# Optimization experiments

Hardware: AMD Instinct MI355X
Metric: run time of the kernel (lower is better)

The kernel has to match this reference:

```python
import jax, jax.numpy as jnp
import numpy as np

NUM_NODES = 1_200_000
NUM_FILLER = 200_000
NUM_PHYS = NUM_NODES - NUM_FILLER  # 1,000,000 physical nodes
NUM_MOVABLE = 900_000
NBX = NBY = 512
XL, XH, YL, YH = 0.0, 1000.0, 0.0, 1000.0
BSX = (XH - XL) / NBX
BSY = (YH - YL) / NBY
PIN_STRETCH = 1.4142135623730951
UNIT_PIN_CAP = 0.05
MAX_RATE = 1.5
MIN_RATE = 1.0 / MAX_RATE
K = 5  # max bins overlapped per dimension (span<=4.0, bin~1.95)


def _overlap_terms(lo, hi, bin_size, origin, nb):
    # lo, hi: [n] interval per node. Returns bin indices [n,K] and overlap lengths [n,K].
    il = jnp.clip(jnp.floor((lo - origin) / bin_size).astype(jnp.int32), 0, nb - 1)
    idx = il[:, None] + jnp.arange(K, dtype=jnp.int32)[None, :]
    valid = idx < nb
    idx = jnp.clip(idx, 0, nb - 1)
    b_lo = origin + idx.astype(lo.dtype) * bin_size
    ov = jnp.maximum(jnp.minimum(hi[:, None], b_lo + bin_size) - jnp.maximum(lo[:, None], b_lo), 0.0)
    return idx, jnp.where(valid, ov, 0.0)


def _forward(pos, node_size_x, node_size_y, flat_node2pin_start_map):
    P = NUM_PHYS
    sx, sy = node_size_x[:P], node_size_y[:P]
    # stretched half sizes: at least half a stretched bin
    hx = 0.5 * jnp.maximum(BSX * PIN_STRETCH, sx)
    hy = 0.5 * jnp.maximum(BSY * PIN_STRETCH, sy)
    cx = pos[:P] + 0.5 * sx
    cy = pos[NUM_NODES:NUM_NODES + P] + 0.5 * sy
    pw = (flat_node2pin_start_map[1:P + 1] - flat_node2pin_start_map[:P]).astype(pos.dtype)
    density = pw / (4.0 * hx * hy)  # pins per unit area over stretched bbox

    # stage 1: scatter stretched-bbox pin density into bin map
    ix, ovx = _overlap_terms(cx - hx, cx + hx, BSX, XL, NBX)  # [P,K]
    iy, ovy = _overlap_terms(cy - hy, cy + hy, BSY, YL, NBY)  # [P,K]
    contrib = ovx[:, :, None] * ovy[:, None, :] * density[:, None, None]  # [P,K,K]
    flat_idx = (ix[:, :, None] * NBY + iy[:, None, :]).reshape(-1)
    pin_map = jnp.zeros(NBX * NBY, dtype=pos.dtype).at[flat_idx].add(contrib.reshape(-1))

    # stage 2: pin utilization per bin, clamped adjust rate
    util = jnp.clip(pin_map / (BSX * BSY * UNIT_PIN_CAP), MIN_RATE, MAX_RATE)

    # stage 3: per movable node, integrate utilization over its (unstretched) bbox
    M = NUM_MOVABLE
    x_lo = pos[:M]
    x_hi = x_lo + node_size_x[:M]
    y_lo = pos[NUM_NODES:NUM_NODES + M]
    y_hi = y_lo + node_size_y[:M]
    jx, wx = _overlap_terms(x_lo, x_hi, BSX, XL, NBX)  # [M,K]
    jy, wy = _overlap_terms(y_lo, y_hi, BSY, YL, NBY)  # [M,K]
    u = util[jx[:, :, None] * NBY + jy[:, None, :]]  # [M,K,K]
    instance_pin_area = jnp.sum(wx[:, :, None] * wy[:, None, :] * u, axis=(1, 2))
    return instance_pin_area


def setup_inputs() -> dict:
    key = jax.random.key(0)
    k1, k2, k3, k4 = jax.random.split(key, 4)
    node_size_x = jax.random.uniform(k1, (NUM_NODES,), jnp.float32, 1.0, 4.0)
    node_size_y = jnp.full((NUM_NODES,), 2.0, jnp.float32)  # row height
    px = jax.random.uniform(k2, (NUM_NODES,), jnp.float32, 0.0, 995.0)
    py = jax.random.uniform(k3, (NUM_NODES,), jnp.float32, 0.0, 995.0)
    pos = jnp.concatenate([px, py])
    pin_counts = jax.random.randint(k4, (NUM_PHYS,), 1, 9, jnp.int32)
    flat = jnp.concatenate([jnp.zeros(1, jnp.int32), jnp.cumsum(pin_counts).astype(jnp.int32)])
    return {"pos": pos, "node_size_x": node_size_x, "node_size_y": node_size_y,
            "flat_node2pin_start_map": flat}


def reference(pos, node_size_x, node_size_y, flat_node2pin_start_map):
    return _forward(pos, node_size_x, node_size_y, flat_node2pin_start_map)
```

## Files before the change

### kernel.cpp

```cpp
#include <hip/hip_runtime.h>

#define NUM_NODES   1200000
#define NUM_FILLER  200000
#define NUM_PHYS    (NUM_NODES - NUM_FILLER)
#define NUM_MOVABLE 900000
#define NBX 512
#define NBY 512
#define NBINS (NBX * NBY)
#define BSX 1.953125f
#define BSY 1.953125f
#define PIN_STRETCH 1.4142135623730951f
#define CAP 0.19073486328125f
#define INV_CAP (1.0f / 0.19073486328125f)
#define MAX_RATE 1.5f
#define MIN_RATE (1.0f/1.5f)
#define K 5

#define HYC (0.5f * fmaxf(BSY * PIN_STRETCH, 2.0f))

#define NT2     512
#define TROW    16
#define TCOL    32
#define HALO    (K - 1)
#define LROW    (TROW + HALO)
#define LCOL    (TCOL + HALO)
#define SBLK    1024
#define NPB     2048
#define NBLK    ((NUM_PHYS + NPB - 1) / NPB)

__device__ __forceinline__ int bin_lo(float lo) {
    int il = (int)floorf(lo / BSX);
    return min(max(il, 0), NBX - 1);
}

__device__ __forceinline__ int tile_of(int il, int jl) {
    return ((il >> 4) << 4) | (jl >> 5);
}

__global__ __launch_bounds__(SBLK, 8) void sort_phys(
    const float* __restrict__ pos,
    const float* __restrict__ nsx,
    const int*   __restrict__ flat,
    int2*        __restrict__ meta,
    float4*      __restrict__ rec,
    float*       __restrict__ pin)
{
    __shared__ int    cnt[NT2];
    __shared__ int    lofs[NT2];
    __shared__ int    wsum[8];
    __shared__ int    totalS;
    __shared__ float4 stage[NPB];
    int tid = threadIdx.x;
    int bid = blockIdx.x;
    if (tid < NT2) cnt[tid] = 0;
    for (int i = bid * SBLK + tid; i < NBINS; i += NBLK * SBLK)
        pin[i] = 0.0f;
    __syncthreads();

    int q = bid * SBLK + tid;
    bool valid = (2 * q + 1) < NUM_PHYS;
    float4 r2[2];
    int tl[2] = {-1, -1};
    if (valid) {
        float2 px = ((const float2*)pos)[q];
        float2 py = ((const float2*)(pos + NUM_NODES))[q];
        float2 sx = ((const float2*)nsx)[q];
        int2 f2 = ((const int2*)flat)[q];
        int f3 = flat[2 * q + 2];
        float pxs[2] = {px.x, px.y};
        float pys[2] = {py.x, py.y};
        float sxs[2] = {sx.x, sx.y};
        int   pws[2] = {f2.y - f2.x, f3 - f2.y};
        #pragma unroll
        for (int j = 0; j < 2; ++j) {
            float hx = 0.5f * fmaxf(BSX * PIN_STRETCH, sxs[j]);
            float cx = pxs[j] + 0.5f * sxs[j];
            float cy = pys[j] + 0.5f * 2.0f;
            float d  = (float)pws[j] / (4.0f * hx * HYC);
            r2[j] = make_float4(cx, cy, hx, d);
            int t = tile_of(bin_lo(cx - hx), bin_lo(cy - HYC));
            tl[j] = t;
            atomicAdd(&cnt[t], 1);
        }
    }
    __syncthreads();

    int lane = tid & 63, wid = tid >> 6;
    int v = (tid < NT2) ? cnt[tid] : 0;
    #pragma unroll
    for (int off = 1; off < 64; off <<= 1) {
        int u = __shfl_up(v, off, 64);
        if (lane >= off) v += u;
    }
    if (wid < 8 && lane == 63) wsum[wid] = v;
    __syncthreads();
    if (tid == 0) {
        int run = 0;
        #pragma unroll
        for (int w = 0; w < 8; ++w) { int c = wsum[w]; wsum[w] = run; run += c; }
        totalS = run;
    }
    __syncthreads();
    if (tid < NT2) {
        int inc = v + wsum[wid];
        int e = inc - cnt[tid];
        lofs[tid] = e;
        meta[(size_t)bid * NT2 + tid] = make_int2(cnt[tid], e);
    }
    __syncthreads();

    if (valid) {
        #pragma unroll
        for (int j = 0; j < 2; ++j) {
            int r = atomicAdd(&lofs[tl[j]], 1);
            stage[r] = r2[j];
        }
    }
    __syncthreads();

    int total = totalS;
    float4* __restrict__ dst = rec + (size_t)bid * NPB;
    for (int k = tid; k < total; k += SBLK)
        dst[k] = stage[k];
}

__global__ __launch_bounds__(1024, 8) void accumulate_tiles(
    const float4* __restrict__ rec,
    const int2*   __restrict__ meta,
    float*        __restrict__ pin)
{
    __shared__ float tileA[LROW * LCOL];
    __shared__ int offB[NBLK];
    __shared__ int prefB[NBLK + 1];
    __shared__ int wsum[8];
    int tid = threadIdx.x;
    int t = blockIdx.x;
    int bx0 = (t >> 4) * TROW, by0 = (t & 15) * TCOL;

    if (tid < LROW * LCOL) tileA[tid] = 0.0f;
    int c = 0;
    if (tid < NBLK) {
        int2 m = meta[(size_t)tid * NT2 + t];
        c = m.x;
        offB[tid] = m.y;
    }
    int lane = tid & 63, wid = tid >> 6;
    int v = c;
    #pragma unroll
    for (int off = 1; off < 64; off <<= 1) {
        int u = __shfl_up(v, off, 64);
        if (lane >= off) v += u;
    }
    if (wid < 8 && lane == 63) wsum[wid] = v;
    __syncthreads();
    if (tid == 0) {
        int run = 0;
        #pragma unroll
        for (int w = 0; w < 8; ++w) { int cc = wsum[w]; wsum[w] = run; run += cc; }
        prefB[0] = 0;
    }
    __syncthreads();
    if (tid < NBLK) prefB[tid + 1] = v + wsum[wid];
    __syncthreads();

    int total = prefB[NBLK];
    for (int k = tid; k < total; k += 1024) {
        int lo = 0, hi = NBLK;
        while (hi - lo > 1) {
            int mid = (lo + hi) >> 1;
            if (k >= prefB[mid]) lo = mid; else hi = mid;
        }
        float4 r = rec[(size_t)lo * NPB + offB[lo] + (k - prefB[lo])];
        float cx = r.x, cy = r.y, hx = r.z, d = r.w;
        float lox = cx - hx, hix = cx + hx;
        float loy = cy - HYC, hiy = cy + HYC;
        int il = bin_lo(lox), jl = bin_lo(loy);
        int ie = min(min((int)floorf(hix / BSX), NBX - 1), il + HALO);
        int je = min(min((int)floorf(hiy / BSY), NBY - 1), jl + HALO);
        int lr = il - bx0, lc = jl - by0;
        for (int a = il; a <= ie; ++a) {
            float blo = (float)a * BSX;
            float ox = fmaxf(fminf(hix, blo + BSX) - fmaxf(lox, blo), 0.0f);
            int rowb = (lr + (a - il)) * LCOL + lc;
            for (int b2 = jl; b2 <= je; ++b2) {
                float blo2 = (float)b2 * BSY;
                float oy = fmaxf(fminf(hiy, blo2 + BSY) - fmaxf(loy, blo2), 0.0f);
                float cc = ox * oy * d;
                if (cc != 0.0f) atomicAdd(&tileA[rowb + (b2 - jl)], cc);
            }
        }
    }
    __syncthreads();
    if (tid < LROW * LCOL) {
        float v2 = tileA[tid];
        int r = tid / LCOL, cc = tid % LCOL;
        int gx = bx0 + r, gy = by0 + cc;
        if (gx < NBX && gy < NBY) {
            bool interior = (r >= HALO) && (r < TROW) && (cc >= HALO) && (cc < TCOL);
            if (interior) {
                if (v2 != 0.0f) pin[gx * NBY + gy] = v2;
            } else {
                if (v2 != 0.0f) atomicAdd(&pin[gx * NBY + gy], v2);
            }
        }
    }
}

__global__ __launch_bounds__(256) void gather_pin_area(
    const float* __restrict__ pos,
    const float* __restrict__ nsx,
    const float* __restrict__ pin,
    float*       __restrict__ out)
{
    int q = blockIdx.x * blockDim.x + threadIdx.x;
    if (q >= NUM_MOVABLE / 2) return;

    float2 xl2 = ((const float2*)pos)[q];
    float2 yl2 = ((const float2*)(pos + NUM_NODES))[q];
    float2 sx2 = ((const float2*)nsx)[q];

    float xls[2] = {xl2.x, xl2.y};
    float yls[2] = {yl2.x, yl2.y};
    float sxs[2] = {sx2.x, sx2.y};
    float res[2];

    #pragma unroll
    for (int j = 0; j < 2; ++j) {
        float xlo = xls[j], xhi = xlo + sxs[j];
        float ylo = yls[j], yhi = ylo + 2.0f;
        int xb = min(bin_lo(xlo), NBX - 4);
        int yb = min(bin_lo(ylo), NBY - 3);

        float u[4][3];
        #pragma unroll
        for (int a = 0; a < 4; ++a) {
            const float* __restrict__ row = pin + (xb + a) * NBY + yb;
            u[a][0] = row[0]; u[a][1] = row[1]; u[a][2] = row[2];
        }
        float wx[4], wy[3];
        #pragma unroll
        for (int kx = 0; kx < 4; ++kx) {
            float blo = (float)(xb + kx) * BSX;
            wx[kx] = fmaxf(fminf(xhi, blo + BSX) - fmaxf(xlo, blo), 0.0f);
        }
        #pragma unroll
        for (int ky = 0; ky < 3; ++ky) {
            float blo = (float)(yb + ky) * BSY;
            wy[ky] = fmaxf(fminf(yhi, blo + BSY) - fmaxf(ylo, blo), 0.0f);
        }
        float acc = 0.0f;
        #pragma unroll
        for (int a = 0; a < 4; ++a)
            #pragma unroll
            for (int b = 0; b < 3; ++b) {
                float uc = fminf(fmaxf(u[a][b] * INV_CAP, MIN_RATE), MAX_RATE);
                acc += wx[a] * wy[b] * uc;
            }
        res[j] = acc;
    }
    ((float2*)out)[q] = make_float2(res[0], res[1]);
}

__global__ __launch_bounds__(256) void scatter_pin_map_agent(
    const float* __restrict__ pos,
    const float* __restrict__ nsx,
    const float* __restrict__ nsy,
    const int*   __restrict__ flat,
    float*       __restrict__ map)
{
    int p = blockIdx.x * blockDim.x + threadIdx.x;
    if (p >= NUM_PHYS) return;
    float sx = nsx[p], sy = nsy[p];
    float hx = 0.5f * fmaxf(BSX * PIN_STRETCH, sx);
    float hy = 0.5f * fmaxf(BSY * PIN_STRETCH, sy);
    float cx = pos[p] + 0.5f * sx;
    float cy = pos[NUM_NODES + p] + 0.5f * sy;
    float pw = (float)(flat[p + 1] - flat[p]);
    float density = pw / (4.0f * hx * hy);
    float lox = cx - hx, hixv = cx + hx;
    float loy = cy - hy, hiyv = cy + hy;
    int il = bin_lo(lox), jl = bin_lo(loy);
    int ie = min(min((int)floorf(hixv / BSX), NBX - 1), il + K - 1);
    int je = min(min((int)floorf(hiyv / BSY), NBY - 1), jl + K - 1);
    for (int a = il; a <= ie; ++a) {
        float blo = (float)a * BSX;
        float ox = fmaxf(fminf(hixv, blo + BSX) - fmaxf(lox, blo), 0.0f);
        for (int b = jl; b <= je; ++b) {
            float blo2 = (float)b * BSY;
            float oy = fmaxf(fminf(hiyv, blo2 + BSY) - fmaxf(loy, blo2), 0.0f);
            float c = ox * oy * density;
            if (c != 0.0f) atomicAdd(&map[a * NBY + b], c);
        }
    }
}

__global__ __launch_bounds__(256) void gather_general(
    const float* __restrict__ pos,
    const float* __restrict__ nsx,
    const float* __restrict__ nsy,
    const float* __restrict__ pin,
    float*       __restrict__ out)
{
    int m = blockIdx.x * blockDim.x + threadIdx.x;
    if (m >= NUM_MOVABLE) return;
    float xlo = pos[m];
    float xhi = xlo + nsx[m];
    float ylo = pos[NUM_NODES + m];
    float yhi = ylo + nsy[m];
    int il = bin_lo(xlo);
    int ie = min(min((int)floorf(xhi / BSX), NBX - 1), il + K - 1);
    int jl = bin_lo(ylo);
    int je = min(min((int)floorf(yhi / BSY), NBY - 1), jl + K - 1);
    float acc = 0.0f;
    for (int a = il; a <= ie; ++a) {
        float blo = (float)a * BSX;
        float wxv = fmaxf(fminf(xhi, blo + BSX) - fmaxf(xlo, blo), 0.0f);
        const float* __restrict__ row = pin + a * NBY;
        for (int b2 = jl; b2 <= je; ++b2) {
            float blo2 = (float)b2 * BSY;
            float wyv = fmaxf(fminf(yhi, blo2 + BSY) - fmaxf(ylo, blo2), 0.0f);
            float uc = fminf(fmaxf(row[b2] * INV_CAP, MIN_RATE), MAX_RATE);
            acc += wxv * wyv * uc;
        }
    }
    out[m] = acc;
}

extern "C" void kernel_launch(void* const* d_in, const int* in_sizes, int n_in,
                              void* d_out, int out_size, void* d_ws, size_t ws_size,
                              hipStream_t stream) {
    const float* pos  = (const float*)d_in[0];
    const float* nsx  = (const float*)d_in[1];
    const float* nsy  = (const float*)d_in[2];
    const int*   flat = (const int*)d_in[3];
    float* out = (float*)d_out;

    char* wsb = (char*)d_ws;
    float*  pin  = (float*)wsb;
    int2*   meta = (int2*)(wsb + (size_t)NBINS * 4);
    float4* rec  = (float4*)(wsb + (size_t)NBINS * 4
                             + (size_t)NBLK * NT2 * 8);
    size_t needed = (size_t)NBINS * 4 + (size_t)NBLK * NT2 * 8
                  + (size_t)NBLK * NPB * 16;

    dim3 blk(256);
    if (ws_size >= needed) {
        sort_phys<<<NBLK, dim3(SBLK), 0, stream>>>(pos, nsx, flat,
                                                   meta, rec, pin);
        accumulate_tiles<<<NT2, dim3(1024), 0, stream>>>(rec, meta, pin);
        gather_pin_area<<<(NUM_MOVABLE / 2 + 255) / 256, blk, 0, stream>>>(pos, nsx, pin, out);
    } else {
        hipMemsetAsync(pin, 0, (size_t)NBINS * 4, stream);
        scatter_pin_map_agent<<<(NUM_PHYS + 255) / 256, blk, 0, stream>>>(pos, nsx, nsy, flat, pin);
        gather_general<<<(NUM_MOVABLE + 255) / 256, blk, 0, stream>>>(pos, nsx, nsy, pin, out);
    }
}
```

Baseline: 133.5 us.

## Fuse sort, tile accumulation and gather into one cooperative persistent kernel

Replaces the three-kernel pipeline (sort_phys, accumulate_tiles, gather_pin_area) with a single cooperative kernel of 512 blocks x 512 threads that separates the stages with grid.sync(). Each block now bins about 1954 nodes instead of 2048 so the block count matches the tile count, and it reuses one shared buffer for both the staging records and the tile patch. The aim is to remove launch gaps and inter-kernel drain between three short kernels. The cost is the grid-wide barriers, 512-thread blocks with fewer threads in flight, and a grid-stride gather loop. It falls back to the general path if the cooperative launch fails.

```diff
diff --git a/kernel.cpp b/kernel.cpp
--- a/kernel.cpp
+++ b/kernel.cpp
@@ -1,8 +1,10 @@
 #include <hip/hip_runtime.h>
+#include <hip/hip_cooperative_groups.h>
+
+namespace cg = cooperative_groups;
 
 #define NUM_NODES   1200000
-#define NUM_FILLER  200000
-#define NUM_PHYS    (NUM_NODES - NUM_FILLER)
+#define NUM_PHYS    1000000
 #define NUM_MOVABLE 900000
 #define NBX 512
 #define NBY 512
@@ -10,23 +12,24 @@
 #define BSX 1.953125f
 #define BSY 1.953125f
 #define PIN_STRETCH 1.4142135623730951f
-#define CAP 0.19073486328125f
 #define INV_CAP (1.0f / 0.19073486328125f)
 #define MAX_RATE 1.5f
 #define MIN_RATE (1.0f/1.5f)
 #define K 5
+#define HALO (K - 1)
 
 #define HYC (0.5f * fmaxf(BSY * PIN_STRETCH, 2.0f))
 
-#define NT2     512
-#define TROW    16
-#define TCOL    32
-#define HALO    (K - 1)
-#define LROW    (TROW + HALO)
-#define LCOL    (TCOL + HALO)
-#define SBLK    1024
-#define NPB     2048
-#define NBLK    ((NUM_PHYS + NPB - 1) / NPB)
+#define GRID 512
+#define BLK  512
+#define NT2  512
+#define TROW 16
+#define TCOL 32
+#define LROW (TROW + HALO)
+#define LCOL (TCOL + HALO)
+#define NPAIRS (NUM_PHYS / 2)
+#define PPB ((NPAIRS + GRID - 1) / GRID)
+#define RSTR (2 * PPB)
 
 __device__ __forceinline__ int bin_lo(float lo) {
     int il = (int)floorf(lo / BSX);
@@ -37,62 +40,72 @@
     return ((il >> 4) << 4) | (jl >> 5);
 }
 
-__global__ __launch_bounds__(SBLK, 8) void sort_phys(
+__global__ __launch_bounds__(BLK, 4) void fused_pipeline(
     const float* __restrict__ pos,
     const float* __restrict__ nsx,
     const int*   __restrict__ flat,
     int2*        __restrict__ meta,
     float4*      __restrict__ rec,
-    float*       __restrict__ pin)
+    float*       __restrict__ pin,
+    float*       __restrict__ out)
 {
-    __shared__ int    cnt[NT2];
-    __shared__ int    lofs[NT2];
-    __shared__ int    wsum[8];
-    __shared__ int    totalS;
-    __shared__ float4 stage[NPB];
-    int tid = threadIdx.x;
-    int bid = blockIdx.x;
-    if (tid < NT2) cnt[tid] = 0;
-    for (int i = bid * SBLK + tid; i < NBINS; i += NBLK * SBLK)
-        pin[i] = 0.0f;
-    __syncthreads();
-
-    int q = bid * SBLK + tid;
-    bool valid = (2 * q + 1) < NUM_PHYS;
-    float4 r2[2];
-    int tl[2] = {-1, -1};
-    if (valid) {
-        float2 px = ((const float2*)pos)[q];
-        float2 py = ((const float2*)(pos + NUM_NODES))[q];
-        float2 sx = ((const float2*)nsx)[q];
-        int2 f2 = ((const int2*)flat)[q];
-        int f3 = flat[2 * q + 2];
-        float pxs[2] = {px.x, px.y};
-        float pys[2] = {py.x, py.y};
-        float sxs[2] = {sx.x, sx.y};
-        int   pws[2] = {f2.y - f2.x, f3 - f2.y};
-        #pragma unroll
-        for (int j = 0; j < 2; ++j) {
-            float hx = 0.5f * fmaxf(BSX * PIN_STRETCH, sxs[j]);
-            float cx = pxs[j] + 0.5f * sxs[j];
-            float cy = pys[j] + 0.5f * 2.0f;
-            float d  = (float)pws[j] / (4.0f * hx * HYC);
-            r2[j] = make_float4(cx, cy, hx, d);
-            int t = tile_of(bin_lo(cx - hx), bin_lo(cy - HYC));
-            tl[j] = t;
-            atomicAdd(&cnt[t], 1);
-        }
-    }
-    __syncthreads();
-
-    int lane = tid & 63, wid = tid >> 6;
-    int v = (tid < NT2) ? cnt[tid] : 0;
+    __shared__ __align__(16) char smem[RSTR * 16];
+    __shared__ int cntS[NT2];
+    __shared__ int lofs[NT2];
+    __shared__ int wsum[8];
+    __shared__ int totalS;
+
+    cg::grid_group grid = cg::this_grid();
+    const int tid  = threadIdx.x;
+    const int bid  = blockIdx.x;
+    const int lane = tid & 63;
+    const int wid  = tid >> 6;
+
+    pin[bid * BLK + tid] = 0.0f;
+
+    cntS[tid] = 0;
+    __syncthreads();
+
+    float4* stage = (float4*)smem;
+    const int base = bid * PPB;
+    const int pend = min(base + PPB, NPAIRS);
+    float4 r4[4];
+    int    tl[4] = {-1, -1, -1, -1};
+    #pragma unroll
+    for (int s = 0; s < 2; ++s) {
+        int q = base + s * BLK + tid;
+        if (q < pend) {
+            float2 px = ((const float2*)pos)[q];
+            float2 py = ((const float2*)(pos + NUM_NODES))[q];
+            float2 sx = ((const float2*)nsx)[q];
+            int2   f2 = ((const int2*)flat)[q];
+            int    f3 = flat[2 * q + 2];
+            float pxs[2] = {px.x, px.y};
+            float pys[2] = {py.x, py.y};
+            float sxs[2] = {sx.x, sx.y};
+            int   pws[2] = {f2.y - f2.x, f3 - f2.y};
+            #pragma unroll
+            for (int j = 0; j < 2; ++j) {
+                float hx = 0.5f * fmaxf(BSX * PIN_STRETCH, sxs[j]);
+                float cx = pxs[j] + 0.5f * sxs[j];
+                float cy = pys[j] + 1.0f;
+                float d  = (float)pws[j] / (4.0f * hx * HYC);
+                r4[2 * s + j] = make_float4(cx, cy, hx, d);
+                int t = tile_of(bin_lo(cx - hx), bin_lo(cy - HYC));
+                tl[2 * s + j] = t;
+                atomicAdd(&cntS[t], 1);
+            }
+        }
+    }
+    __syncthreads();
+
+    int v = cntS[tid];
     #pragma unroll
     for (int off = 1; off < 64; off <<= 1) {
         int u = __shfl_up(v, off, 64);
         if (lane >= off) v += u;
     }
-    if (wid < 8 && lane == 63) wsum[wid] = v;
+    if (lane == 63) wsum[wid] = v;
     __syncthreads();
     if (tid == 0) {
         int run = 0;
@@ -101,57 +114,52 @@
         totalS = run;
     }
     __syncthreads();
-    if (tid < NT2) {
+    {
         int inc = v + wsum[wid];
-        int e = inc - cnt[tid];
+        int e = inc - cntS[tid];
         lofs[tid] = e;
-        meta[(size_t)bid * NT2 + tid] = make_int2(cnt[tid], e);
-    }
-    __syncthreads();
-
-    if (valid) {
-        #pragma unroll
-        for (int j = 0; j < 2; ++j) {
-            int r = atomicAdd(&lofs[tl[j]], 1);
-            stage[r] = r2[j];
-        }
-    }
-    __syncthreads();
-
-    int total = totalS;
-    float4* __restrict__ dst = rec + (size_t)bid * NPB;
-    for (int k = tid; k < total; k += SBLK)
-        dst[k] = stage[k];
-}
-
-__global__ __launch_bounds__(1024, 8) void accumulate_tiles(
-    const float4* __restrict__ rec,
-    const int2*   __restrict__ meta,
-    float*        __restrict__ pin)
-{
-    __shared__ float tileA[LROW * LCOL];
-    __shared__ int offB[NBLK];
-    __shared__ int prefB[NBLK + 1];
-    __shared__ int wsum[8];
-    int tid = threadIdx.x;
-    int t = blockIdx.x;
-    int bx0 = (t >> 4) * TROW, by0 = (t & 15) * TCOL;
-
-    if (tid < LROW * LCOL) tileA[tid] = 0.0f;
-    int c = 0;
-    if (tid < NBLK) {
+        meta[(size_t)bid * NT2 + tid] = make_int2(cntS[tid], e);
+    }
+    __syncthreads();
+
+    #pragma unroll
+    for (int r = 0; r < 4; ++r)
+        if (tl[r] >= 0) {
+            int slot = atomicAdd(&lofs[tl[r]], 1);
+            stage[slot] = r4[r];
+        }
+    __syncthreads();
+    {
+        int total = totalS;
+        float4* __restrict__ dst = rec + (size_t)bid * RSTR;
+        for (int k2 = tid; k2 < total; k2 += BLK) dst[k2] = stage[k2];
+    }
+
+    grid.sync();
+
+    float* patch = (float*)smem;
+    int*   offB  = (int*)(smem + LROW * LCOL * 4);
+    int*   prefB = offB + GRID;
+
+    const int t   = bid;
+    const int bx0 = (t >> 4) * TROW;
+    const int by0 = (t & 15) * TCOL;
+
+    for (int i = tid; i < LROW * LCOL; i += BLK) patch[i] = 0.0f;
+
+    int c;
+    {
         int2 m = meta[(size_t)tid * NT2 + t];
         c = m.x;
         offB[tid] = m.y;
     }
-    int lane = tid & 63, wid = tid >> 6;
-    int v = c;
+    int v2 = c;
     #pragma unroll
     for (int off = 1; off < 64; off <<= 1) {
-        int u = __shfl_up(v, off, 64);
-        if (lane >= off) v += u;
-    }
-    if (wid < 8 && lane == 63) wsum[wid] = v;
+        int u = __shfl_up(v2, off, 64);
+        if (lane >= off) v2 += u;
+    }
+    if (lane == 63) wsum[wid] = v2;
     __syncthreads();
     if (tid == 0) {
         int run = 0;
@@ -160,17 +168,17 @@
         prefB[0] = 0;
     }
     __syncthreads();
-    if (tid < NBLK) prefB[tid + 1] = v + wsum[wid];
-    __syncthreads();
-
-    int total = prefB[NBLK];
-    for (int k = tid; k < total; k += 1024) {
-        int lo = 0, hi = NBLK;
+    prefB[tid + 1] = v2 + wsum[wid];
+    __syncthreads();
+
+    int total2 = prefB[GRID];
+    for (int k = tid; k < total2; k += BLK) {
+        int lo = 0, hi = GRID;
         while (hi - lo > 1) {
             int mid = (lo + hi) >> 1;
             if (k >= prefB[mid]) lo = mid; else hi = mid;
         }
-        float4 r = rec[(size_t)lo * NPB + offB[lo] + (k - prefB[lo])];
+        float4 r = rec[(size_t)lo * RSTR + offB[lo] + (k - prefB[lo])];
         float cx = r.x, cy = r.y, hx = r.z, d = r.w;
         float lox = cx - hx, hix = cx + hx;
         float loy = cy - HYC, hiy = cy + HYC;
@@ -186,79 +194,70 @@
                 float blo2 = (float)b2 * BSY;
                 float oy = fmaxf(fminf(hiy, blo2 + BSY) - fmaxf(loy, blo2), 0.0f);
                 float cc = ox * oy * d;
-                if (cc != 0.0f) atomicAdd(&tileA[rowb + (b2 - jl)], cc);
-            }
-        }
-    }
-    __syncthreads();
-    if (tid < LROW * LCOL) {
-        float v2 = tileA[tid];
-        int r = tid / LCOL, cc = tid % LCOL;
+                if (cc != 0.0f) atomicAdd(&patch[rowb + (b2 - jl)], cc);
+            }
+        }
+    }
+    __syncthreads();
+    for (int i = tid; i < LROW * LCOL; i += BLK) {
+        float pv = patch[i];
+        int r = i / LCOL, cc = i % LCOL;
         int gx = bx0 + r, gy = by0 + cc;
-        if (gx < NBX && gy < NBY) {
+        if (gx < NBX && gy < NBY && pv != 0.0f) {
             bool interior = (r >= HALO) && (r < TROW) && (cc >= HALO) && (cc < TCOL);
-            if (interior) {
-                if (v2 != 0.0f) pin[gx * NBY + gy] = v2;
-            } else {
-                if (v2 != 0.0f) atomicAdd(&pin[gx * NBY + gy], v2);
-            }
-        }
-    }
-}
-
-__global__ __launch_bounds__(256) void gather_pin_area(
-    const float* __restrict__ pos,
-    const float* __restrict__ nsx,
-    const float* __restrict__ pin,
-    float*       __restrict__ out)
-{
-    int q = blockIdx.x * blockDim.x + threadIdx.x;
-    if (q >= NUM_MOVABLE / 2) return;
-
-    float2 xl2 = ((const float2*)pos)[q];
-    float2 yl2 = ((const float2*)(pos + NUM_NODES))[q];
-    float2 sx2 = ((const float2*)nsx)[q];
-
-    float xls[2] = {xl2.x, xl2.y};
-    float yls[2] = {yl2.x, yl2.y};
-    float sxs[2] = {sx2.x, sx2.y};
-    float res[2];
-
-    #pragma unroll
-    for (int j = 0; j < 2; ++j) {
-        float xlo = xls[j], xhi = xlo + sxs[j];
-        float ylo = yls[j], yhi = ylo + 2.0f;
-        int xb = min(bin_lo(xlo), NBX - 4);
-        int yb = min(bin_lo(ylo), NBY - 3);
-
-        float u[4][3];
+            if (interior) pin[gx * NBY + gy] = pv;
+            else          atomicAdd(&pin[gx * NBY + gy], pv);
+        }
+    }
+
+    grid.sync();
+
+    for (int q = bid * BLK + tid; q < NUM_MOVABLE / 2; q += GRID * BLK) {
+        float2 xl2 = ((const float2*)pos)[q];
+        float2 yl2 = ((const float2*)(pos + NUM_NODES))[q];
+        float2 sx2 = ((const float2*)nsx)[q];
+
+        float xls[2] = {xl2.x, xl2.y};
+        float yls[2] = {yl2.x, yl2.y};
+        float sxs[2] = {sx2.x, sx2.y};
+        float res[2];
+
         #pragma unroll
-        for (int a = 0; a < 4; ++a) {
-            const float* __restrict__ row = pin + (xb + a) * NBY + yb;
-            u[a][0] = row[0]; u[a][1] = row[1]; u[a][2] = row[2];
-        }
-        float wx[4], wy[3];
-        #pragma unroll
-        for (int kx = 0; kx < 4; ++kx) {
-            float blo = (float)(xb + kx) * BSX;
-            wx[kx] = fmaxf(fminf(xhi, blo + BSX) - fmaxf(xlo, blo), 0.0f);
-        }
-        #pragma unroll
-        for (int ky = 0; ky < 3; ++ky) {
-            float blo = (float)(yb + ky) * BSY;
-            wy[ky] = fmaxf(fminf(yhi, blo + BSY) - fmaxf(ylo, blo), 0.0f);
-        }
-        float acc = 0.0f;
-        #pragma unroll
-        for (int a = 0; a < 4; ++a)
-            #pragma unroll
-            for (int b = 0; b < 3; ++b) {
-                float uc = fminf(fmaxf(u[a][b] * INV_CAP, MIN_RATE), MAX_RATE);
-                acc += wx[a] * wy[b] * uc;
-            }
-        res[j] = acc;
-    }
-    ((float2*)out)[q] = make_float2(res[0], res[1]);
+        for (int j = 0; j < 2; ++j) {
+            float xlo = xls[j], xhi = xlo + sxs[j];
+            float ylo = yls[j], yhi = ylo + 2.0f;
+            int xb = min(bin_lo(xlo), NBX - 4);
+            int yb = min(bin_lo(ylo), NBY - 3);
+
+            float u[4][3];
+            #pragma unroll
+            for (int a = 0; a < 4; ++a) {
+                const float* __restrict__ row = pin + (xb + a) * NBY + yb;
+                u[a][0] = row[0]; u[a][1] = row[1]; u[a][2] = row[2];
+            }
+            float wx[4], wy[3];
+            #pragma unroll
+            for (int kx = 0; kx < 4; ++kx) {
+                float blo = (float)(xb + kx) * BSX;
+                wx[kx] = fmaxf(fminf(xhi, blo + BSX) - fmaxf(xlo, blo), 0.0f);
+            }
+            #pragma unroll
+            for (int ky = 0; ky < 3; ++ky) {
+                float blo = (float)(yb + ky) * BSY;
+                wy[ky] = fmaxf(fminf(yhi, blo + BSY) - fmaxf(ylo, blo), 0.0f);
+            }
+            float acc = 0.0f;
+            #pragma unroll
+            for (int a = 0; a < 4; ++a)
+                #pragma unroll
+                for (int b = 0; b < 3; ++b) {
+                    float uc = fminf(fmaxf(u[a][b] * INV_CAP, MIN_RATE), MAX_RATE);
+                    acc += wx[a] * wy[b] * uc;
+                }
+            res[j] = acc;
+        }
+        ((float2*)out)[q] = make_float2(res[0], res[1]);
+    }
 }
 
 __global__ __launch_bounds__(256) void scatter_pin_map_agent(
@@ -339,17 +338,20 @@
     float*  pin  = (float*)wsb;
     int2*   meta = (int2*)(wsb + (size_t)NBINS * 4);
     float4* rec  = (float4*)(wsb + (size_t)NBINS * 4
-                             + (size_t)NBLK * NT2 * 8);
-    size_t needed = (size_t)NBINS * 4 + (size_t)NBLK * NT2 * 8
-                  + (size_t)NBLK * NPB * 16;
-
-    dim3 blk(256);
+                             + (size_t)GRID * NT2 * 8);
+    size_t needed = (size_t)NBINS * 4 + (size_t)GRID * NT2 * 8
+                  + (size_t)GRID * RSTR * 16;
+
+    bool done = false;
     if (ws_size >= needed) {
-        sort_phys<<<NBLK, dim3(SBLK), 0, stream>>>(pos, nsx, flat,
-                                                   meta, rec, pin);
-        accumulate_tiles<<<NT2, dim3(1024), 0, stream>>>(rec, meta, pin);
-        gather_pin_area<<<(NUM_MOVABLE / 2 + 255) / 256, blk, 0, stream>>>(pos, nsx, pin, out);
-    } else {
+        void* args[] = {(void*)&pos, (void*)&nsx, (void*)&flat,
+                        (void*)&meta, (void*)&rec, (void*)&pin, (void*)&out};
+        hipError_t err = hipLaunchCooperativeKernel(
+            (const void*)fused_pipeline, dim3(GRID), dim3(BLK), args, 0, stream);
+        done = (err == hipSuccess);
+    }
+    if (!done) {
+        dim3 blk(256);
         hipMemsetAsync(pin, 0, (size_t)NBINS * 4, stream);
         scatter_pin_map_agent<<<(NUM_PHYS + 255) / 256, blk, 0, stream>>>(pos, nsx, nsy, flat, pin);
         gather_general<<<(NUM_MOVABLE + 255) / 256, blk, 0, stream>>>(pos, nsx, nsy, pin, out);
```

Result: slower. 253.7 us (+90.0%).
